# Kernel optimization log

Hardware: AMD Instinct MI355X
Metric: run time of the kernel (lower is better)

Reference implementation:

```python
import jax, jax.numpy as jnp
import numpy as np


def setup_inputs() -> dict:
    key = jax.random.key(0)
    k1, k2 = jax.random.split(key)
    pc1 = jax.random.normal(k1, (8, 2048, 3), dtype=jnp.float32)
    pc2 = jax.random.normal(k2, (8, 2048, 3), dtype=jnp.float32)
    return {"pc1": pc1, "pc2": pc2}


def reference(pc1, pc2):
    # Flatten to point lists, matching pc.reshape(-1, 3)
    p1 = pc1.reshape(-1, 3)  # [N1, 3]
    p2 = pc2.reshape(-1, 3)  # [N2, 3]
    # Squared pairwise distances via ||a||^2 + ||b||^2 - 2 a.b
    sq1 = jnp.sum(p1 * p1, axis=-1)  # [N1]
    sq2 = jnp.sum(p2 * p2, axis=-1)  # [N2]
    d2 = sq1[:, None] + sq2[None, :] - 2.0 * jnp.einsum('nd,md->nm', p1, p2)  # [N1, N2]
    d2 = jnp.maximum(d2, 0.0)
    d = jnp.sqrt(d2)  # Euclidean, matching cKDTree.query distances
    # dist1 = NN distance from each pc2 point into pc1 (tree1.query(pc2))
    dist1 = jnp.min(d, axis=0)  # [N2]
    # dist2 = NN distance from each pc1 point into pc2 (tree2.query(pc1))
    dist2 = jnp.min(d, axis=1)  # [N1]
    return jnp.mean(dist1) + jnp.mean(dist2)
```

## Files before the change

kernel.cpp:

```cpp
#include <hip/hip_runtime.h>
#include <math.h>

#define N_PTS 16384
#define TPB   256
#define IP    8
#define ROWS_B (TPB * IP)
#define IBLK  (N_PTS / ROWS_B)
#define JT    128
#define JS    (N_PTS / JT)
#define NCH   (JT / 2)
#define REDB  64

__global__ __launch_bounds__(TPB) void chamfer_init(
    unsigned int* __restrict__ dmin, float* __restrict__ outp) {
  int id = blockIdx.x * TPB + threadIdx.x;
  dmin[id] = 0x7F800000u;
  if (id == 0) outp[0] = 0.f;
}

__global__ __launch_bounds__(TPB, 4) void chamfer_min(
    const float* __restrict__ p1, const float* __restrict__ p2,
    unsigned int* __restrict__ dmin) {
  __shared__ float4 tile[JT];
  __shared__ unsigned int cmin[JT];

  const int jbase = blockIdx.x * JT;
  for (int t = threadIdx.x; t < JT; t += TPB) {
    float x = p2[3 * (jbase + t) + 0];
    float y = p2[3 * (jbase + t) + 1];
    float z = p2[3 * (jbase + t) + 2];
    tile[t] = make_float4(x, y, z, 0.5f * (x * x + y * y + z * z));
    cmin[t] = 0x7F800000u;
  }

  const int ibase = blockIdx.y * ROWS_B;
  float nx[IP], ny[IP], nz[IP], h[IP], rmin[IP];
#pragma unroll
  for (int m = 0; m < IP; ++m) {
    int r = ibase + m * TPB + threadIdx.x;
    float x = p1[3 * r + 0], y = p1[3 * r + 1], z = p1[3 * r + 2];
    nx[m] = -x; ny[m] = -y; nz[m] = -z;
    h[m] = 0.5f * (x * x + y * y + z * z);
    rmin[m] = INFINITY;
  }
  __syncthreads();

  const int base = (threadIdx.x & 63) + ((threadIdx.x >> 6) << 4);
#pragma unroll 2
  for (int s = 0; s < NCH; ++s) {
    const int pos = (base + s) & (NCH - 1);
    float4 qa = tile[pos];
    float4 qb = tile[pos + NCH];
    float cpa = INFINITY, cpb = INFINITY;
#pragma unroll
    for (int m = 0; m < IP; m += 2) {
      float ta = h[m] + qa.w;
      ta = fmaf(nx[m], qa.x, ta); ta = fmaf(ny[m], qa.y, ta); ta = fmaf(nz[m], qa.z, ta);
      float tb = h[m] + qb.w;
      tb = fmaf(nx[m], qb.x, tb); tb = fmaf(ny[m], qb.y, tb); tb = fmaf(nz[m], qb.z, tb);
      float ua = h[m + 1] + qa.w;
      ua = fmaf(nx[m + 1], qa.x, ua); ua = fmaf(ny[m + 1], qa.y, ua); ua = fmaf(nz[m + 1], qa.z, ua);
      float ub = h[m + 1] + qb.w;
      ub = fmaf(nx[m + 1], qb.x, ub); ub = fmaf(ny[m + 1], qb.y, ub); ub = fmaf(nz[m + 1], qb.z, ub);
      asm("v_min3_f32 %0, %1, %2, %3" : "=v"(rmin[m])     : "v"(ta), "v"(tb), "v"(rmin[m]));
      asm("v_min3_f32 %0, %1, %2, %3" : "=v"(rmin[m + 1]) : "v"(ua), "v"(ub), "v"(rmin[m + 1]));
      asm("v_min3_f32 %0, %1, %2, %3" : "=v"(cpa)         : "v"(ta), "v"(ua), "v"(cpa));
      asm("v_min3_f32 %0, %1, %2, %3" : "=v"(cpb)         : "v"(tb), "v"(ub), "v"(cpb));
    }
    atomicMin(&cmin[pos],       __float_as_uint(fmaxf(cpa, 0.f)));
    atomicMin(&cmin[pos + NCH], __float_as_uint(fmaxf(cpb, 0.f)));
  }

#pragma unroll
  for (int m = 0; m < IP; ++m) {
    float d2 = fmaxf(0.f, 2.f * rmin[m]);
    atomicMin(&dmin[ibase + m * TPB + threadIdx.x], __float_as_uint(d2));
  }

  __syncthreads();
  for (int t = threadIdx.x; t < JT; t += TPB) {
    float v = __uint_as_float(cmin[t]);
    atomicMin(&dmin[N_PTS + jbase + t], __float_as_uint(2.f * v));
  }
}

__global__ __launch_bounds__(TPB) void chamfer_reduce(
    const unsigned int* __restrict__ dmin, float* __restrict__ outp) {
  float s = 0.f;
  for (int i = blockIdx.x * TPB + threadIdx.x; i < 2 * N_PTS; i += REDB * TPB)
    s += sqrtf(__uint_as_float(dmin[i]));
#pragma unroll
  for (int off = 32; off > 0; off >>= 1)
    s += __shfl_down(s, off, 64);
  __shared__ float partial[TPB / 64];
  if ((threadIdx.x & 63) == 0) partial[threadIdx.x >> 6] = s;
  __syncthreads();
  if (threadIdx.x == 0) {
    float t = 0.f;
    for (int w = 0; w < TPB / 64; ++w) t += partial[w];
    atomicAdd(outp, t * (1.0f / (float)N_PTS));
  }
}

extern "C" void kernel_launch(void* const* d_in, const int* in_sizes, int n_in,
                              void* d_out, int out_size, void* d_ws, size_t ws_size,
                              hipStream_t stream) {
  const float* pc1 = (const float*)d_in[0];
  const float* pc2 = (const float*)d_in[1];
  unsigned int* dmin = (unsigned int*)d_ws;

  chamfer_init<<<(2 * N_PTS) / TPB, TPB, 0, stream>>>(dmin, (float*)d_out);
  chamfer_min<<<dim3(JS, IBLK), TPB, 0, stream>>>(pc1, pc2, dmin);
  chamfer_reduce<<<REDB, TPB, 0, stream>>>(dmin, (float*)d_out);
}
```

Measured before the change: 91.08 us.

## Rotate column-min accumulators across lanes via ds_bpermute instead of LDS atomics

Each step previously ended with two LDS atomicMin calls to record per-column minima. Now each lane passes its running column-min to its neighbour with ds_bpermute, so the accumulator follows the column as the lanes rotate through the tile. Only one pair of atomics per lane is issued after the loop. The tile load for the next step is also prefetched into registers before the current compute. This trades LDS atomic traffic for cross-lane permutes and a few extra live registers.

Result: no change. 90.76 us (-0.4%).

```diff
diff --git a/kernel.cpp b/kernel.cpp
--- a/kernel.cpp
+++ b/kernel.cpp
@@ -45,30 +45,44 @@
   }
   __syncthreads();
 
-  const int base = (threadIdx.x & 63) + ((threadIdx.x >> 6) << 4);
+  const int lane = threadIdx.x & 63;
+  const int base = lane + ((threadIdx.x >> 6) << 4);
+  const int nxtb = ((lane + 1) & 63) << 2;
+
+  float Aa = INFINITY, Ab = INFINITY;
+  const int pini = base & (NCH - 1);
+  float4 qa = tile[pini];
+  float4 qb = tile[pini + NCH];
 #pragma unroll 2
   for (int s = 0; s < NCH; ++s) {
-    const int pos = (base + s) & (NCH - 1);
-    float4 qa = tile[pos];
-    float4 qb = tile[pos + NCH];
-    float cpa = INFINITY, cpb = INFINITY;
+    float cpa = __int_as_float(__builtin_amdgcn_ds_bpermute(nxtb, __float_as_int(Aa)));
+    float cpb = __int_as_float(__builtin_amdgcn_ds_bpermute(nxtb, __float_as_int(Ab)));
+    float4 ca = qa, cb = qb;
+    const int pn = (base + s + 1) & (NCH - 1);
+    qa = tile[pn];
+    qb = tile[pn + NCH];
 #pragma unroll
     for (int m = 0; m < IP; m += 2) {
-      float ta = h[m] + qa.w;
-      ta = fmaf(nx[m], qa.x, ta); ta = fmaf(ny[m], qa.y, ta); ta = fmaf(nz[m], qa.z, ta);
-      float tb = h[m] + qb.w;
-      tb = fmaf(nx[m], qb.x, tb); tb = fmaf(ny[m], qb.y, tb); tb = fmaf(nz[m], qb.z, tb);
-      float ua = h[m + 1] + qa.w;
-      ua = fmaf(nx[m + 1], qa.x, ua); ua = fmaf(ny[m + 1], qa.y, ua); ua = fmaf(nz[m + 1], qa.z, ua);
-      float ub = h[m + 1] + qb.w;
-      ub = fmaf(nx[m + 1], qb.x, ub); ub = fmaf(ny[m + 1], qb.y, ub); ub = fmaf(nz[m + 1], qb.z, ub);
+      float ta = h[m] + ca.w;
+      ta = fmaf(nx[m], ca.x, ta); ta = fmaf(ny[m], ca.y, ta); ta = fmaf(nz[m], ca.z, ta);
+      float tb = h[m] + cb.w;
+      tb = fmaf(nx[m], cb.x, tb); tb = fmaf(ny[m], cb.y, tb); tb = fmaf(nz[m], cb.z, tb);
+      float ua = h[m + 1] + ca.w;
+      ua = fmaf(nx[m + 1], ca.x, ua); ua = fmaf(ny[m + 1], ca.y, ua); ua = fmaf(nz[m + 1], ca.z, ua);
+      float ub = h[m + 1] + cb.w;
+      ub = fmaf(nx[m + 1], cb.x, ub); ub = fmaf(ny[m + 1], cb.y, ub); ub = fmaf(nz[m + 1], cb.z, ub);
       asm("v_min3_f32 %0, %1, %2, %3" : "=v"(rmin[m])     : "v"(ta), "v"(tb), "v"(rmin[m]));
       asm("v_min3_f32 %0, %1, %2, %3" : "=v"(rmin[m + 1]) : "v"(ua), "v"(ub), "v"(rmin[m + 1]));
       asm("v_min3_f32 %0, %1, %2, %3" : "=v"(cpa)         : "v"(ta), "v"(ua), "v"(cpa));
       asm("v_min3_f32 %0, %1, %2, %3" : "=v"(cpb)         : "v"(tb), "v"(ub), "v"(cpb));
     }
-    atomicMin(&cmin[pos],       __float_as_uint(fmaxf(cpa, 0.f)));
-    atomicMin(&cmin[pos + NCH], __float_as_uint(fmaxf(cpb, 0.f)));
+    Aa = cpa; Ab = cpb;
+  }
+
+  {
+    const int pe = (base + NCH - 1) & (NCH - 1);
+    atomicMin(&cmin[pe],       __float_as_uint(fmaxf(Aa, 0.f)));
+    atomicMin(&cmin[pe + NCH], __float_as_uint(fmaxf(Ab, 0.f)));
   }
 
 #pragma unroll
```
